# Performance work log

Hardware: AMD Instinct MI355X
Metric: run time of the kernel (lower is better)

Reference implementation:

```python
import jax, jax.numpy as jnp
import numpy as np

# PyG ChebConv defaults: normalization='sym', lambda_max=2.0.
# L_hat = 2*L/lambda_max - I = (I - D^-1/2 A D^-1/2) - I = -D^-1/2 A D^-1/2
# (self-loop/diagonal coefficient is exactly 0 when lambda_max == 2).

N_NODES = 30000
IN_CH = 128
HID_CH = 256
K = 3
N_EDGES = 480000


def _norm_weights(edge_index, n):
    src, dst = edge_index[0], edge_index[1]
    mask = src != dst  # remove_self_loops
    ones = jnp.where(mask, 1.0, 0.0)
    deg = jax.ops.segment_sum(ones, src, num_segments=n)
    dis = jnp.where(deg > 0, deg ** -0.5, 0.0)  # deg_inv_sqrt, inf -> 0
    w = jnp.where(mask, -dis[src] * dis[dst], 0.0)  # -A_sym edge weights
    return src, dst, w


def _cheb_conv(x, src, dst, w, W, b, n):
    # Tx_0 = x; Tx_1 = L_hat x; Tx_k = 2 L_hat Tx_{k-1} - Tx_{k-2}
    def lap(h):  # sparse matvec: (L_hat h)[i] = sum_{e: dst_e=i} w_e * h[src_e]
        return jax.ops.segment_sum(w[:, None] * h[src], dst, num_segments=n)

    Tx_prev = x
    out = x @ W[0]
    if W.shape[0] > 1:
        Tx_cur = lap(x)
        out = out + Tx_cur @ W[1]
        for k in range(2, W.shape[0]):
            Tx_next = 2.0 * lap(Tx_cur) - Tx_prev
            out = out + Tx_next @ W[k]
            Tx_prev, Tx_cur = Tx_cur, Tx_next
    return out + b


def setup_inputs() -> dict:
    key = jax.random.key(0)
    k1, k2, k3, k4, k5, k6 = jax.random.split(key, 6)
    x = jax.random.normal(k1, (N_NODES, IN_CH), dtype=jnp.float32)
    edge_index = jax.random.randint(k2, (2, N_EDGES), 0, N_NODES, dtype=jnp.int64)
    s1 = (1.0 / (IN_CH * K)) ** 0.5
    s2 = (1.0 / (HID_CH * K)) ** 0.5
    W1 = jax.random.uniform(k3, (K, IN_CH, HID_CH), jnp.float32, -s1, s1)
    b1 = jax.random.uniform(k4, (HID_CH,), jnp.float32, -s1, s1)
    W2 = jax.random.uniform(k5, (K, HID_CH, IN_CH), jnp.float32, -s2, s2)
    b2 = jax.random.uniform(k6, (IN_CH,), jnp.float32, -s2, s2)
    return {"x": x, "edge_index": edge_index, "W1": W1, "b1": b1, "W2": W2, "b2": b2}


def reference(x, edge_index, W1, b1, W2, b2):
    n = x.shape[0]
    src, dst, w = _norm_weights(edge_index, n)
    h = jax.nn.relu(_cheb_conv(x, src, dst, w, W1, b1, n))
    return _cheb_conv(h, src, dst, w, W2, b2, n)
```

## Files before the change

kernel.cpp:

```cpp
#include <hip/hip_runtime.h>
#include <hip/hip_bf16.h>


#define ELLW 64

typedef short bf16x8_t __attribute__((ext_vector_type(8)));
typedef unsigned short u16x4_t __attribute__((ext_vector_type(4)));
typedef unsigned short u16x8_t __attribute__((ext_vector_type(8)));
typedef float f32x4_t __attribute__((ext_vector_type(4)));

static __device__ inline unsigned short f2bf(float f) {
    __hip_bfloat16 h = __float2bfloat16(f);
    return __builtin_bit_cast(unsigned short, h);
}
static __device__ inline float bfbits2f(unsigned int lo16) {
    unsigned int u = lo16 << 16;
    return __builtin_bit_cast(float, u);
}

__global__ __launch_bounds__(256) void build_prep_kernel(
        const int* __restrict__ src, const int* __restrict__ dst,
        int* __restrict__ degi, int* __restrict__ cnt,
        unsigned short* __restrict__ ell, int E, int gB,
        const float* __restrict__ W1, const float* __restrict__ W2,
        const float* __restrict__ x,
        unsigned short* __restrict__ Bt1, unsigned short* __restrict__ Bt2,
        unsigned short* __restrict__ xb, int nx4) {
    int bid = blockIdx.x;
    if (bid < gB) {
        int e = bid * 256 + threadIdx.x;
        if (e >= E) return;
        int s = src[e], d = dst[e];
        if (s != d) atomicAdd(&degi[s], 1);
        int pos = atomicAdd(&cnt[d], 1);
        if (pos < ELLW) ell[(size_t)d * ELLW + pos] = (unsigned short)s;
        return;
    }
    const int NB1 = 256 * 384, NB2 = 384 * 256;
    int i = (bid - gB) * 256 + threadIdx.x;
    if (i < NB1) {
        int n = i / 384, k = i % 384;
        Bt1[(size_t)n * 384 + k] = f2bf(W1[(size_t)k * 256 + n]);
    } else if (i < NB1 + NB2) {
        int j = i - NB1;
        int n = j / 256, k = j % 256;
        float v;
        if (n < 128) v = W2[(size_t)(1 * 256 + k) * 128 + n];
        else if (n < 256) v = W2[(size_t)(2 * 256 + k) * 128 + (n - 128)];
        else v = W2[(size_t)k * 128 + (n - 256)] - W2[(size_t)(2 * 256 + k) * 128 + (n - 256)];
        Bt2[(size_t)n * 256 + k] = f2bf(v);
    } else {
        int j = i - NB1 - NB2;
        if (j < nx4) {
            f32x4_t v = *(const f32x4_t*)&x[(size_t)j * 4];
            u16x4_t u;
            u.x = f2bf(v.x); u.y = f2bf(v.y); u.z = f2bf(v.z); u.w = f2bf(v.w);
            *(u16x4_t*)&xb[(size_t)j * 4] = u;
        }
    }
}

__global__ __launch_bounds__(256) void lap_ell_kernel(const unsigned short* __restrict__ Xb,
                                                      float* __restrict__ Yf,
                                                      unsigned short* __restrict__ Yb,
                                                      const int* __restrict__ cnt,
                                                      const unsigned short* __restrict__ ell,
                                                      const int* __restrict__ degi,
                                                      const unsigned short* __restrict__ add,
                                                      const float* __restrict__ bias,
                                                      float s, float a, int N) {
    int wave = threadIdx.x >> 6;
    int lane = threadIdx.x & 63;
    int node = blockIdx.x * 4 + wave;
    if (node >= N) return;
    int n = cnt[node];
    if (n > ELLW) n = ELLW;
    int dn = degi[node];
    float fdn = (float)dn;
    const unsigned short* row = ell + (size_t)node * ELLW;

    float ax0 = 0.f, ay0 = 0.f, ax1 = 0.f, ay1 = 0.f;
    float ax2 = 0.f, ay2 = 0.f, ax3 = 0.f, ay3 = 0.f;
    int j = 0;
    for (; j + 4 <= n; j += 4) {
        u16x4_t s4 = *(const u16x4_t*)&row[j];
        int s0 = __builtin_amdgcn_readfirstlane((int)s4.x);
        int s1 = __builtin_amdgcn_readfirstlane((int)s4.y);
        int s2 = __builtin_amdgcn_readfirstlane((int)s4.z);
        int s3 = __builtin_amdgcn_readfirstlane((int)s4.w);
        unsigned int v0 = *(const unsigned int*)&Xb[(size_t)s0 * 128 + lane * 2];
        unsigned int v1 = *(const unsigned int*)&Xb[(size_t)s1 * 128 + lane * 2];
        unsigned int v2 = *(const unsigned int*)&Xb[(size_t)s2 * 128 + lane * 2];
        unsigned int v3 = *(const unsigned int*)&Xb[(size_t)s3 * 128 + lane * 2];
        int d0 = degi[s0], d1 = degi[s1], d2 = degi[s2], d3 = degi[s3];
        float w0 = (s0 != node && dn > 0 && d0 > 0) ? -rsqrtf(fdn * (float)d0) : 0.0f;
        float w1 = (s1 != node && dn > 0 && d1 > 0) ? -rsqrtf(fdn * (float)d1) : 0.0f;
        float w2 = (s2 != node && dn > 0 && d2 > 0) ? -rsqrtf(fdn * (float)d2) : 0.0f;
        float w3 = (s3 != node && dn > 0 && d3 > 0) ? -rsqrtf(fdn * (float)d3) : 0.0f;
        ax0 = fmaf(w0, bfbits2f(v0 & 0xffffu), ax0);
        ay0 = fmaf(w0, bfbits2f(v0 >> 16), ay0);
        ax1 = fmaf(w1, bfbits2f(v1 & 0xffffu), ax1);
        ay1 = fmaf(w1, bfbits2f(v1 >> 16), ay1);
        ax2 = fmaf(w2, bfbits2f(v2 & 0xffffu), ax2);
        ay2 = fmaf(w2, bfbits2f(v2 >> 16), ay2);
        ax3 = fmaf(w3, bfbits2f(v3 & 0xffffu), ax3);
        ay3 = fmaf(w3, bfbits2f(v3 >> 16), ay3);
    }
    for (; j < n; ++j) {
        int s0 = __builtin_amdgcn_readfirstlane((int)row[j]);
        unsigned int v0 = *(const unsigned int*)&Xb[(size_t)s0 * 128 + lane * 2];
        int d0 = degi[s0];
        float w0 = (s0 != node && dn > 0 && d0 > 0) ? -rsqrtf(fdn * (float)d0) : 0.0f;
        ax0 = fmaf(w0, bfbits2f(v0 & 0xffffu), ax0);
        ay0 = fmaf(w0, bfbits2f(v0 >> 16), ay0);
    }
    float rx = s * ((ax0 + ax1) + (ax2 + ax3));
    float ry = s * ((ay0 + ay1) + (ay2 + ay3));
    size_t o = (size_t)node * 128 + lane * 2;
    if (add) {
        unsigned int ad = *(const unsigned int*)&add[o];
        rx = fmaf(a, bfbits2f(ad & 0xffffu), rx);
        ry = fmaf(a, bfbits2f(ad >> 16), ry);
    }
    if (bias) {
        rx += bias[lane * 2];
        ry += bias[lane * 2 + 1];
    }
    if (Yf) {
        float2 r; r.x = rx; r.y = ry;
        *(float2*)&Yf[o] = r;
    }
    if (Yb) {
        unsigned int ob = ((unsigned int)f2bf(ry) << 16) | f2bf(rx);
        *(unsigned int*)&Yb[o] = ob;
    }
}

__global__ __launch_bounds__(512) void gemm_mfma_kernel(
        const unsigned short* __restrict__ A0, const unsigned short* __restrict__ A1,
        const unsigned short* __restrict__ A2, int ldA,
        const unsigned short* __restrict__ Bt, int K,
        unsigned short* __restrict__ Ob0, unsigned short* __restrict__ Ob1,
        unsigned short* __restrict__ Ob2,
        int ldO, const float* __restrict__ bias, int M, int relu) {
    __shared__ unsigned short As[128][72];
    __shared__ unsigned short Bs[64][72];

    int tid = threadIdx.x;
    int lane = tid & 63;
    int wid = tid >> 6;
    int wm = wid >> 1;
    int wn = wid & 1;
    int lm = lane & 15, lg = lane >> 4;

    int rowBase = blockIdx.x * 128;
    int colBase = blockIdx.y * 64;

    f32x4_t acc[2][2] = {};

    for (int k0 = 0; k0 < K; k0 += 64) {
        int seg = k0 >> 7;
        int acol = k0 & 127;
        const unsigned short* A = (seg == 0) ? A0 : ((seg == 1) ? A1 : A2);

        {
            int row = tid >> 2;
            int c = (tid & 3) * 16;
            int gr = rowBase + row;
            u16x8_t v0 = {0, 0, 0, 0, 0, 0, 0, 0};
            u16x8_t v1 = {0, 0, 0, 0, 0, 0, 0, 0};
            if (gr < M) {
                const unsigned short* ap = &A[(size_t)gr * ldA + acol + c];
                v0 = *(const u16x8_t*)ap;
                v1 = *(const u16x8_t*)(ap + 8);
            }
            *(u16x8_t*)&As[row][c] = v0;
            *(u16x8_t*)&As[row][c + 8] = v1;
        }
        {
            int n = tid >> 3;
            int kb = tid & 7;
            u16x8_t bv = *(const u16x8_t*)&Bt[(size_t)(colBase + n) * K + k0 + kb * 8];
            *(u16x8_t*)&Bs[n][kb * 8] = bv;
        }
        __syncthreads();

#pragma unroll
        for (int ks = 0; ks < 2; ++ks) {
            int koff = ks * 32 + lg * 8;
            bf16x8_t a0 = *(const bf16x8_t*)&As[wm * 32 + lm][koff];
            bf16x8_t a1 = *(const bf16x8_t*)&As[wm * 32 + 16 + lm][koff];
            bf16x8_t b0 = *(const bf16x8_t*)&Bs[wn * 32 + lm][koff];
            bf16x8_t b1 = *(const bf16x8_t*)&Bs[wn * 32 + 16 + lm][koff];
            acc[0][0] = __builtin_amdgcn_mfma_f32_16x16x32_bf16(a0, b0, acc[0][0], 0, 0, 0);
            acc[0][1] = __builtin_amdgcn_mfma_f32_16x16x32_bf16(a0, b1, acc[0][1], 0, 0, 0);
            acc[1][0] = __builtin_amdgcn_mfma_f32_16x16x32_bf16(a1, b0, acc[1][0], 0, 0, 0);
            acc[1][1] = __builtin_amdgcn_mfma_f32_16x16x32_bf16(a1, b1, acc[1][1], 0, 0, 0);
        }
        __syncthreads();
    }

    int oseg = colBase >> 7;
    unsigned short* Ob = (oseg == 0) ? Ob0 : ((oseg == 1) ? Ob1 : Ob2);
    int lcbase = (colBase & 127) + wn * 32;
#pragma unroll
    for (int i = 0; i < 2; ++i) {
#pragma unroll
        for (int j = 0; j < 2; ++j) {
            int lc = lcbase + j * 16 + lm;
            int gcol = colBase + wn * 32 + j * 16 + lm;
            float bval = bias ? bias[gcol] : 0.0f;
#pragma unroll
            for (int r = 0; r < 4; ++r) {
                int gr = rowBase + wm * 32 + i * 16 + lg * 4 + r;
                if (gr < M) {
                    float v = acc[i][j][r] + bval;
                    if (relu) v = fmaxf(v, 0.0f);
                    Ob[(size_t)gr * ldO + lc] = f2bf(v);
                }
            }
        }
    }
}

extern "C" void kernel_launch(void* const* d_in, const int* in_sizes, int n_in,
                              void* d_out, int out_size, void* d_ws, size_t ws_size,
                              hipStream_t stream) {
    const float* x  = (const float*)d_in[0];
    const int*   ei = (const int*)d_in[1];
    const float* W1 = (const float*)d_in[2];
    const float* b1 = (const float*)d_in[3];
    const float* W2 = (const float*)d_in[4];
    const float* b2 = (const float*)d_in[5];
    float* out = (float*)d_out;

    const int IN = 128, HID = 256;
    int N = in_sizes[0] / IN;
    int E = in_sizes[1] / 2;
    const int* src = ei;
    const int* dst = ei + E;

    char* ws = (char*)d_ws;
    size_t off = 0;
    auto alloc = [&](size_t bytes) -> void* {
        void* p = ws + off;
        off += (bytes + 255) & ~(size_t)255;
        return p;
    };
    int* ibuf   = (int*)alloc((size_t)2 * N * 4);
    int* degi   = ibuf;
    int* cnt    = ibuf + N;
    unsigned short* ell = (unsigned short*)alloc((size_t)N * ELLW * 2);
    unsigned short* xb  = (unsigned short*)alloc((size_t)N * IN * 2);
    unsigned short* T1b = (unsigned short*)alloc((size_t)N * IN * 2);
    unsigned short* T2b = (unsigned short*)alloc((size_t)N * IN * 2);
    unsigned short* A2b = (unsigned short*)alloc((size_t)N * IN * 2);
    unsigned short* Ib  = (unsigned short*)alloc((size_t)N * IN * 2);
    unsigned short* hb  = (unsigned short*)alloc((size_t)N * HID * 2);
    unsigned short* Db  = (unsigned short*)alloc((size_t)N * IN * 2);
    unsigned short* Zb  = (unsigned short*)alloc((size_t)N * IN * 2);
    unsigned short* Bt1 = (unsigned short*)alloc((size_t)256 * 384 * 2);
    unsigned short* Bt2 = (unsigned short*)alloc((size_t)384 * 256 * 2);

    int gLap = (N + 3) / 4;
    int gBlkM = (N + 127) / 128;
    int nx4 = N * IN / 4;
    int gB = (E + 255) / 256;
    int gP = (256 * 384 + 384 * 256 + nx4 + 255) / 256;

    hipMemsetAsync(ibuf, 0, (size_t)2 * N * 4, stream);
    build_prep_kernel<<<gB + gP, 256, 0, stream>>>(src, dst, degi, cnt, ell, E, gB,
                                                   W1, W2, x, Bt1, Bt2, xb, nx4);

    lap_ell_kernel<<<gLap, 256, 0, stream>>>(xb, nullptr, T1b, cnt, ell, degi,
                                             nullptr, nullptr, 1.0f, 0.0f, N);
    lap_ell_kernel<<<gLap, 256, 0, stream>>>(T1b, nullptr, T2b, cnt, ell, degi,
                                             xb, nullptr, 2.0f, -1.0f, N);
    {
        dim3 grid(gBlkM, 4);
        gemm_mfma_kernel<<<grid, 512, 0, stream>>>(xb, T1b, T2b, IN,
                                                   Bt1, 384,
                                                   hb, hb + 128, nullptr,
                                                   HID, b1, N, 1);
    }

    {
        dim3 grid(gBlkM, 6);
        gemm_mfma_kernel<<<grid, 512, 0, stream>>>(hb, hb + 128, nullptr, HID,
                                                   Bt2, 256,
                                                   Db, A2b, Zb,
                                                   IN, nullptr, N, 0);
        lap_ell_kernel<<<gLap, 256, 0, stream>>>(A2b, nullptr, Ib, cnt, ell, degi,
                                                 Db, nullptr, 2.0f, 1.0f, N);
        lap_ell_kernel<<<gLap, 256, 0, stream>>>(Ib, out, nullptr, cnt, ell, degi,
                                                 Zb, b2, 1.0f, 1.0f, N);
    }
}
```

Before: 204.4 us.

## Widen GEMM column tile to 128 and unroll sparse gather by eight

The sparse Laplacian gather now processes eight neighbours per iteration with eight independent accumulators, which puts more loads in flight. It also hoists the node's own rsqrt so each edge weight costs one rsqrt and a multiply. The MFMA GEMM tile grows from 128x64 to 128x128, so each wave computes 2x4 output fragments and the column grid is halved. That cuts how often the A tile is reloaded, at the cost of more registers and LDS and fewer blocks.

```diff
diff --git a/kernel.cpp b/kernel.cpp
--- a/kernel.cpp
+++ b/kernel.cpp
@@ -76,46 +76,51 @@
     int n = cnt[node];
     if (n > ELLW) n = ELLW;
     int dn = degi[node];
-    float fdn = (float)dn;
+    float rn = (dn > 0) ? rsqrtf((float)dn) : 0.0f;
     const unsigned short* row = ell + (size_t)node * ELLW;
 
-    float ax0 = 0.f, ay0 = 0.f, ax1 = 0.f, ay1 = 0.f;
-    float ax2 = 0.f, ay2 = 0.f, ax3 = 0.f, ay3 = 0.f;
+    float ax[8], ay[8];
+#pragma unroll
+    for (int k = 0; k < 8; ++k) { ax[k] = 0.0f; ay[k] = 0.0f; }
+
     int j = 0;
-    for (; j + 4 <= n; j += 4) {
+    for (; j + 8 <= n; j += 8) {
+        u16x8_t s8 = *(const u16x8_t*)&row[j];
+#pragma unroll
+        for (int k = 0; k < 8; ++k) {
+            int sk = __builtin_amdgcn_readfirstlane((int)s8[k]);
+            unsigned int v = *(const unsigned int*)&Xb[(size_t)sk * 128 + lane * 2];
+            int dsk = degi[sk];
+            float wk = (sk != node && dsk > 0) ? -rn * rsqrtf((float)dsk) : 0.0f;
+            ax[k] = fmaf(wk, bfbits2f(v & 0xffffu), ax[k]);
+            ay[k] = fmaf(wk, bfbits2f(v >> 16), ay[k]);
+        }
+    }
+    if (j + 4 <= n) {
         u16x4_t s4 = *(const u16x4_t*)&row[j];
-        int s0 = __builtin_amdgcn_readfirstlane((int)s4.x);
-        int s1 = __builtin_amdgcn_readfirstlane((int)s4.y);
-        int s2 = __builtin_amdgcn_readfirstlane((int)s4.z);
-        int s3 = __builtin_amdgcn_readfirstlane((int)s4.w);
-        unsigned int v0 = *(const unsigned int*)&Xb[(size_t)s0 * 128 + lane * 2];
-        unsigned int v1 = *(const unsigned int*)&Xb[(size_t)s1 * 128 + lane * 2];
-        unsigned int v2 = *(const unsigned int*)&Xb[(size_t)s2 * 128 + lane * 2];
-        unsigned int v3 = *(const unsigned int*)&Xb[(size_t)s3 * 128 + lane * 2];
-        int d0 = degi[s0], d1 = degi[s1], d2 = degi[s2], d3 = degi[s3];
-        float w0 = (s0 != node && dn > 0 && d0 > 0) ? -rsqrtf(fdn * (float)d0) : 0.0f;
-        float w1 = (s1 != node && dn > 0 && d1 > 0) ? -rsqrtf(fdn * (float)d1) : 0.0f;
-        float w2 = (s2 != node && dn > 0 && d2 > 0) ? -rsqrtf(fdn * (float)d2) : 0.0f;
-        float w3 = (s3 != node && dn > 0 && d3 > 0) ? -rsqrtf(fdn * (float)d3) : 0.0f;
-        ax0 = fmaf(w0, bfbits2f(v0 & 0xffffu), ax0);
-        ay0 = fmaf(w0, bfbits2f(v0 >> 16), ay0);
-        ax1 = fmaf(w1, bfbits2f(v1 & 0xffffu), ax1);
-        ay1 = fmaf(w1, bfbits2f(v1 >> 16), ay1);
-        ax2 = fmaf(w2, bfbits2f(v2 & 0xffffu), ax2);
-        ay2 = fmaf(w2, bfbits2f(v2 >> 16), ay2);
-        ax3 = fmaf(w3, bfbits2f(v3 & 0xffffu), ax3);
-        ay3 = fmaf(w3, bfbits2f(v3 >> 16), ay3);
+#pragma unroll
+        for (int k = 0; k < 4; ++k) {
+            int sk = __builtin_amdgcn_readfirstlane((int)s4[k]);
+            unsigned int v = *(const unsigned int*)&Xb[(size_t)sk * 128 + lane * 2];
+            int dsk = degi[sk];
+            float wk = (sk != node && dsk > 0) ? -rn * rsqrtf((float)dsk) : 0.0f;
+            ax[k] = fmaf(wk, bfbits2f(v & 0xffffu), ax[k]);
+            ay[k] = fmaf(wk, bfbits2f(v >> 16), ay[k]);
+        }
+        j += 4;
     }
     for (; j < n; ++j) {
-        int s0 = __builtin_amdgcn_readfirstlane((int)row[j]);
-        unsigned int v0 = *(const unsigned int*)&Xb[(size_t)s0 * 128 + lane * 2];
-        int d0 = degi[s0];
-        float w0 = (s0 != node && dn > 0 && d0 > 0) ? -rsqrtf(fdn * (float)d0) : 0.0f;
-        ax0 = fmaf(w0, bfbits2f(v0 & 0xffffu), ax0);
-        ay0 = fmaf(w0, bfbits2f(v0 >> 16), ay0);
-    }
-    float rx = s * ((ax0 + ax1) + (ax2 + ax3));
-    float ry = s * ((ay0 + ay1) + (ay2 + ay3));
+        int sk = __builtin_amdgcn_readfirstlane((int)row[j]);
+        unsigned int v = *(const unsigned int*)&Xb[(size_t)sk * 128 + lane * 2];
+        int dsk = degi[sk];
+        float wk = (sk != node && dsk > 0) ? -rn * rsqrtf((float)dsk) : 0.0f;
+        ax[0] = fmaf(wk, bfbits2f(v & 0xffffu), ax[0]);
+        ay[0] = fmaf(wk, bfbits2f(v >> 16), ay[0]);
+    }
+    float rx = s * (((ax[0] + ax[1]) + (ax[2] + ax[3])) +
+                    ((ax[4] + ax[5]) + (ax[6] + ax[7])));
+    float ry = s * (((ay[0] + ay[1]) + (ay[2] + ay[3])) +
+                    ((ay[4] + ay[5]) + (ay[6] + ay[7])));
     size_t o = (size_t)node * 128 + lane * 2;
     if (add) {
         unsigned int ad = *(const unsigned int*)&add[o];
@@ -144,7 +149,7 @@
         unsigned short* __restrict__ Ob2,
         int ldO, const float* __restrict__ bias, int M, int relu) {
     __shared__ unsigned short As[128][72];
-    __shared__ unsigned short Bs[64][72];
+    __shared__ unsigned short Bs[128][72];
 
     int tid = threadIdx.x;
     int lane = tid & 63;
@@ -154,9 +159,9 @@
     int lm = lane & 15, lg = lane >> 4;
 
     int rowBase = blockIdx.x * 128;
-    int colBase = blockIdx.y * 64;
-
-    f32x4_t acc[2][2] = {};
+    int colBase = blockIdx.y * 128;
+
+    f32x4_t acc[2][4] = {};
 
     for (int k0 = 0; k0 < K; k0 += 64) {
         int seg = k0 >> 7;
@@ -178,10 +183,13 @@
             *(u16x8_t*)&As[row][c + 8] = v1;
         }
         {
-            int n = tid >> 3;
-            int kb = tid & 7;
-            u16x8_t bv = *(const u16x8_t*)&Bt[(size_t)(colBase + n) * K + k0 + kb * 8];
-            *(u16x8_t*)&Bs[n][kb * 8] = bv;
+            int n = tid >> 2;
+            int kb = (tid & 3) * 16;
+            const unsigned short* bp = &Bt[(size_t)(colBase + n) * K + k0 + kb];
+            u16x8_t b0 = *(const u16x8_t*)bp;
+            u16x8_t b1 = *(const u16x8_t*)(bp + 8);
+            *(u16x8_t*)&Bs[n][kb] = b0;
+            *(u16x8_t*)&Bs[n][kb + 8] = b1;
         }
         __syncthreads();
 
@@ -190,25 +198,30 @@
             int koff = ks * 32 + lg * 8;
             bf16x8_t a0 = *(const bf16x8_t*)&As[wm * 32 + lm][koff];
             bf16x8_t a1 = *(const bf16x8_t*)&As[wm * 32 + 16 + lm][koff];
-            bf16x8_t b0 = *(const bf16x8_t*)&Bs[wn * 32 + lm][koff];
-            bf16x8_t b1 = *(const bf16x8_t*)&Bs[wn * 32 + 16 + lm][koff];
+            bf16x8_t b0 = *(const bf16x8_t*)&Bs[wn * 64 + lm][koff];
+            bf16x8_t b1 = *(const bf16x8_t*)&Bs[wn * 64 + 16 + lm][koff];
+            bf16x8_t b2 = *(const bf16x8_t*)&Bs[wn * 64 + 32 + lm][koff];
+            bf16x8_t b3 = *(const bf16x8_t*)&Bs[wn * 64 + 48 + lm][koff];
             acc[0][0] = __builtin_amdgcn_mfma_f32_16x16x32_bf16(a0, b0, acc[0][0], 0, 0, 0);
             acc[0][1] = __builtin_amdgcn_mfma_f32_16x16x32_bf16(a0, b1, acc[0][1], 0, 0, 0);
+            acc[0][2] = __builtin_amdgcn_mfma_f32_16x16x32_bf16(a0, b2, acc[0][2], 0, 0, 0);
+            acc[0][3] = __builtin_amdgcn_mfma_f32_16x16x32_bf16(a0, b3, acc[0][3], 0, 0, 0);
             acc[1][0] = __builtin_amdgcn_mfma_f32_16x16x32_bf16(a1, b0, acc[1][0], 0, 0, 0);
             acc[1][1] = __builtin_amdgcn_mfma_f32_16x16x32_bf16(a1, b1, acc[1][1], 0, 0, 0);
+            acc[1][2] = __builtin_amdgcn_mfma_f32_16x16x32_bf16(a1, b2, acc[1][2], 0, 0, 0);
+            acc[1][3] = __builtin_amdgcn_mfma_f32_16x16x32_bf16(a1, b3, acc[1][3], 0, 0, 0);
         }
         __syncthreads();
     }
 
-    int oseg = colBase >> 7;
+    int oseg = blockIdx.y;
     unsigned short* Ob = (oseg == 0) ? Ob0 : ((oseg == 1) ? Ob1 : Ob2);
-    int lcbase = (colBase & 127) + wn * 32;
 #pragma unroll
     for (int i = 0; i < 2; ++i) {
 #pragma unroll
-        for (int j = 0; j < 2; ++j) {
-            int lc = lcbase + j * 16 + lm;
-            int gcol = colBase + wn * 32 + j * 16 + lm;
+        for (int j = 0; j < 4; ++j) {
+            int lc = wn * 64 + j * 16 + lm;
+            int gcol = colBase + lc;
             float bval = bias ? bias[gcol] : 0.0f;
 #pragma unroll
             for (int r = 0; r < 4; ++r) {
@@ -277,7 +290,7 @@
     lap_ell_kernel<<<gLap, 256, 0, stream>>>(T1b, nullptr, T2b, cnt, ell, degi,
                                              xb, nullptr, 2.0f, -1.0f, N);
     {
-        dim3 grid(gBlkM, 4);
+        dim3 grid(gBlkM, 2);
         gemm_mfma_kernel<<<grid, 512, 0, stream>>>(xb, T1b, T2b, IN,
                                                    Bt1, 384,
                                                    hb, hb + 128, nullptr,
@@ -285,7 +298,7 @@
     }
 
     {
-        dim3 grid(gBlkM, 6);
+        dim3 grid(gBlkM, 3);
         gemm_mfma_kernel<<<grid, 512, 0, stream>>>(hb, hb + 128, nullptr, HID,
                                                    Bt2, 256,
                                                    Db, A2b, Zb,
```

Result: faster. 187.2 us (-8.4%).
